# Kernel optimization log

Measured on AMD Instinct MI355X. Metric: run time of the kernel, lower is better.

The kernel has to match this reference:

```python
import jax, jax.numpy as jnp
import numpy as np

B, C, H, W, HEADS = 16, 256, 64, 64, 4
BN_EPS = 1e-5


def setup_inputs() -> dict:
    key = jax.random.key(0)
    ks = jax.random.split(key, 6)
    sc = lambda k, shape, s: (jax.random.normal(k, shape, jnp.float32) * s)
    return {
        "x": sc(ks[0], (B, C, H, W), 1.0),
        "qkv_w": sc(ks[1], (C, C), C ** -0.5),
        "temp": jnp.ones((HEADS, 1), jnp.float32),
        "proj_w": sc(ks[2], (C, C), C ** -0.5),
        "proj_b": jnp.zeros((C,), jnp.float32),
        "conv1_w": sc(ks[3], (2 * C, C), C ** -0.5),
        "bn1_g": jnp.ones((2 * C,), jnp.float32),
        "bn1_b": jnp.zeros((2 * C,), jnp.float32),
        "bn1_m": jnp.zeros((2 * C,), jnp.float32),
        "bn1_v": jnp.ones((2 * C,), jnp.float32),
        "conv2_w": sc(ks[4], (C, 2 * C), (2 * C) ** -0.5),
        "bn2_g": jnp.ones((C,), jnp.float32),
        "bn2_b": jnp.zeros((C,), jnp.float32),
        "bn2_m": jnp.zeros((C,), jnp.float32),
        "bn2_v": jnp.ones((C,), jnp.float32),
    }


def _attention_tssa(x3, qkv_w, temp, proj_w, proj_b):
    # x3: [b, n, c]
    b, n, c = x3.shape
    d = c // HEADS
    w = (x3 @ qkv_w.T).reshape(b, n, HEADS, d).transpose(0, 2, 1, 3)  # b h n d
    # F.normalize over token dim (dim=-2), eps=1e-12
    nrm = jnp.sqrt(jnp.sum(w * w, axis=2, keepdims=True))
    w_normed = w / jnp.maximum(nrm, 1e-12)
    # logits [b, h, n]; temp is (h, 1) -> broadcast per head
    s = jnp.sum(w_normed * w_normed, axis=-1) * temp[:, 0][None, :, None]
    Pi = jax.nn.softmax(s, axis=1)  # softmax over HEAD dim (torch Softmax(dim=1))
    Pi_n = Pi / (jnp.sum(Pi, axis=-1, keepdims=True) + 1e-8)
    dots = jnp.einsum('bhn,bhnd->bhd', Pi_n, w * w)  # [b, h, d]
    attn = 1.0 / (1.0 + dots)
    out = -(w * Pi[..., None]) * attn[:, :, None, :]  # b h n d
    out = out.transpose(0, 2, 1, 3).reshape(b, n, c)
    return out @ proj_w.T + proj_b


def _bn(y, g, b_, m, v):
    scale = (g / jnp.sqrt(v + BN_EPS))[None, :, None, None]
    return (y - m[None, :, None, None]) * scale + b_[None, :, None, None]


def reference(x, qkv_w, temp, proj_w, proj_b, conv1_w, bn1_g, bn1_b, bn1_m, bn1_v,
              conv2_w, bn2_g, bn2_b, bn2_m, bn2_v):
    b, c, h, w_ = x.shape
    x3 = x.reshape(b, c, h * w_).transpose(0, 2, 1)  # b n c
    a = _attention_tssa(x3, qkv_w, temp, proj_w, proj_b)  # b n c
    x = x + a.transpose(0, 2, 1).reshape(b, c, h, w_)
    # FFN: 1x1 conv -> BN -> SiLU -> 1x1 conv -> BN (no act), residual
    y = jnp.einsum('bchw,oc->bohw', x, conv1_w)
    y = _bn(y, bn1_g, bn1_b, bn1_m, bn1_v)
    y = y * jax.nn.sigmoid(y)  # SiLU
    z = jnp.einsum('bchw,oc->bohw', y, conv2_w)
    z = _bn(z, bn2_g, bn2_b, bn2_m, bn2_v)
    return x + z
```

## Files before the change

### kernel.cpp

```cpp
#include <hip/hip_runtime.h>
#include <hip/hip_bf16.h>
#include <stdint.h>

typedef unsigned short u16;
using bf16x8 = __attribute__((ext_vector_type(8))) short;
using f32x4  = __attribute__((ext_vector_type(4))) float;

#define DEVI static __device__ __forceinline__
#define AS1 __attribute__((address_space(1)))
#define AS3 __attribute__((address_space(3)))

constexpr int CB = 16;
constexpr int CC = 256;
constexpr int CN = 4096;
constexpr int CH = 4;

DEVI u16 f2b(float f){
  union { float f; uint32_t u; } v; v.f = f;
  return (u16)((v.u + 0x7FFFu + ((v.u >> 16) & 1u)) >> 16);
}
DEVI float b2f(u16 u){
  union { uint32_t u; float f; } v; v.u = ((uint32_t)u) << 16; return v.f;
}

__global__ __launch_bounds__(256) void k_prep_w(const float* __restrict__ qkv, const float* __restrict__ pj,
    const float* __restrict__ c1, const float* __restrict__ c2,
    u16* __restrict__ qkvb, u16* __restrict__ pjb, u16* __restrict__ c1b, u16* __restrict__ c2b){
  int id = blockIdx.x * 256 + threadIdx.x;
  if (id < 65536) qkvb[id] = f2b(qkv[id]);
  else if (id < 131072) pjb[id - 65536] = f2b(pj[id - 65536]);
  else if (id < 262144) c1b[id - 131072] = f2b(c1[id - 131072]);
  else c2b[id - 262144] = f2b(c2[id - 262144]);
}

__global__ __launch_bounds__(256) void k_prep_bn(const float* __restrict__ g1,const float* __restrict__ b1,
    const float* __restrict__ m1,const float* __restrict__ v1,
    const float* __restrict__ g2,const float* __restrict__ b2,
    const float* __restrict__ m2,const float* __restrict__ v2,
    float* __restrict__ s1,float* __restrict__ o1,float* __restrict__ s2,float* __restrict__ o2){
  int id = blockIdx.x*256 + threadIdx.x;
  if (id < 512){ float s = g1[id] * rsqrtf(v1[id] + 1e-5f); s1[id] = s; o1[id] = b1[id] - m1[id]*s; }
  else if (id < 768){ int c = id - 512; float s = g2[c] * rsqrtf(v2[c] + 1e-5f); s2[c] = s; o2[c] = b2[c] - m2[c]*s; }
}

__global__ __launch_bounds__(256) void k_tr(const float* __restrict__ x, u16* __restrict__ xb){
  __shared__ float t[32][33];
  int b = blockIdx.x, c0 = blockIdx.y*32, n0 = blockIdx.z*32;
  int tr = threadIdx.x >> 5, tc = threadIdx.x & 31;
  const float* xp = x + ((size_t)b*CC + c0)*CN + n0;
  #pragma unroll
  for (int p=0;p<4;p++) t[tr + p*8][tc] = xp[(size_t)(tr + p*8)*CN + tc];
  __syncthreads();
  u16* op = xb + ((size_t)b*CN + n0)*CC + c0;
  #pragma unroll
  for (int p=0;p<4;p++) op[(size_t)(tr + p*8)*CC + tc] = f2b(t[tc][tr + p*8]);
}

template<int M_, int K_, int EPI>
__global__ __launch_bounds__(256) void k_gemm(
    const u16* __restrict__ Aw, const u16* __restrict__ Act,
    float* of, u16* __restrict__ ob,
    const float* __restrict__ e0, const float* __restrict__ e1,
    const u16* __restrict__ eb)
{
  __shared__ __align__(16) u16 As[2][128*64];
  __shared__ __align__(16) u16 Bs[2][128*64];
  const int t = threadIdx.x;
  const int lane = t & 63, wave = t >> 6;
  const int wr = wave >> 1, wc = wave & 1;
  const int lg = lane >> 4, lr = lane & 15;
  const int gx = gridDim.x, gy = gridDim.y;
  const int nwg = gx * gy * gridDim.z;
  const int id0 = blockIdx.x + gx*(blockIdx.y + gy*blockIdx.z);
  const int id  = (id0 & 7)*(nwg >> 3) + (id0 >> 3);
  const int bx = id % gx; const int rem = id / gx;
  const int by = rem % gy; const int bz = rem / gy;
  const int n0 = bx * 128, m0 = by * 128, b = bz;
  const u16* Ag = Aw + (size_t)m0 * K_;
  const u16* Bg = Act + ((size_t)b * CN + n0) * K_;
  f32x4 acc[4][4] = {};
  constexpr int NT = K_/64;
  int goff[4], ldst[4];
  #pragma unroll
  for (int i=0;i<4;i++){
    int off = (i*256 + t) * 8;
    int m = off >> 6, gq = (off >> 3) & 7;
    int kk = (gq ^ (m & 7)) * 8;
    goff[i] = m*K_ + kk;
    ldst[i] = (i*256 + wave*64)*8;
  }
  auto stage = [&](int p, int kt){
    #pragma unroll
    for (int i=0;i<4;i++){
      __builtin_amdgcn_global_load_lds((AS1 void*)(Ag + goff[i] + kt*64),
                                       (AS3 void*)(&As[p][ldst[i]]), 16, 0, 0);
      __builtin_amdgcn_global_load_lds((AS1 void*)(Bg + goff[i] + kt*64),
                                       (AS3 void*)(&Bs[p][ldst[i]]), 16, 0, 0);
    }
  };
  stage(0, 0);
  stage(1, 1);
  for (int kt = 0; kt < NT; ++kt){
    const int cur = kt & 1;
    if (kt + 1 < NT) { asm volatile("s_waitcnt vmcnt(8)" ::: "memory"); }
    else             { asm volatile("s_waitcnt vmcnt(0)" ::: "memory"); }
    __builtin_amdgcn_s_barrier();
    __builtin_amdgcn_sched_barrier(0);
    bf16x8 af[2][4], bfv[2][4];
    #pragma unroll
    for (int s=0;s<2;s++){
      #pragma unroll
      for (int mi=0;mi<4;mi++){
        int r = wr*64 + mi*16 + lr;
        af[s][mi] = *(const bf16x8*)(&As[cur][r*64 + (((s*4+lg) ^ (r & 7)) * 8)]);
        int r2 = wc*64 + mi*16 + lr;
        bfv[s][mi] = *(const bf16x8*)(&Bs[cur][r2*64 + (((s*4+lg) ^ (r2 & 7)) * 8)]);
      }
    }
    asm volatile("s_waitcnt lgkmcnt(0)" ::: "memory");
    __builtin_amdgcn_sched_barrier(0);
    __builtin_amdgcn_s_barrier();
    if (kt + 2 < NT) stage(cur, kt + 2);
    __builtin_amdgcn_s_setprio(1);
    #pragma unroll
    for (int s=0;s<2;s++)
      #pragma unroll
      for (int mi=0;mi<4;mi++)
        #pragma unroll
        for (int ni=0;ni<4;ni++)
          acc[mi][ni] = __builtin_amdgcn_mfma_f32_16x16x32_bf16(af[s][mi], bfv[s][ni], acc[mi][ni], 0, 0, 0);
    __builtin_amdgcn_s_setprio(0);
  }
  #pragma unroll
  for (int mi=0;mi<4;mi++){
    const int mb = m0 + wr*64 + mi*16 + lg*4;
    float sq[4] = {0.f,0.f,0.f,0.f};
    #pragma unroll
    for (int ni=0;ni<4;ni++){
      const int n = n0 + wc*64 + ni*16 + lr;
      f32x4 v = acc[mi][ni];
      if constexpr (EPI == 0){
        ushort4 u;
        #pragma unroll
        for (int j=0;j<4;j++){ ((u16*)&u)[j] = f2b(v[j]); sq[j] += v[j]*v[j]; }
        *(ushort4*)(ob + ((size_t)b*CN + n)*M_ + mb) = u;
      } else if constexpr (EPI == 1){
        ushort4 u;
        #pragma unroll
        for (int j=0;j<4;j++){
          size_t ix = ((size_t)b*CC + mb + j)*CN + n;
          ((u16*)&u)[j] = f2b(v[j] + e0[mb + j] + e1[ix]);
        }
        *(ushort4*)(ob + ((size_t)b*CN + n)*M_ + mb) = u;
      } else if constexpr (EPI == 2){
        ushort4 u;
        #pragma unroll
        for (int j=0;j<4;j++){
          float r = v[j]*e0[mb+j] + e1[mb+j];
          r = r / (1.f + __expf(-r));
          ((u16*)&u)[j] = f2b(r);
        }
        *(ushort4*)(ob + ((size_t)b*CN + n)*M_ + mb) = u;
      } else {
        ushort4 xw = *(const ushort4*)(eb + ((size_t)b*CN + n)*M_ + mb);
        #pragma unroll
        for (int j=0;j<4;j++){
          size_t ix = ((size_t)b*CC + mb + j)*CN + n;
          of[ix] = v[j]*e0[mb+j] + e1[mb+j] + b2f(((const u16*)&xw)[j]);
        }
      }
    }
    if constexpr (EPI == 0){
      #pragma unroll
      for (int off=1; off<16; off<<=1)
        #pragma unroll
        for (int j=0;j<4;j++) sq[j] += __shfl_xor(sq[j], off);
      if (lr == 0){
        #pragma unroll
        for (int j=0;j<4;j++) atomicAdd(&of[b*CC + mb + j], sq[j]);
      }
    }
  }
}

__global__ __launch_bounds__(256) void k_stats(const u16* __restrict__ W, const float* __restrict__ nrm2,
    const float* __restrict__ temp, float* __restrict__ Pi, float* __restrict__ sumPi,
    float* __restrict__ dotsU){
  __shared__ float red[4][256];
  const int b = blockIdx.x, n0 = blockIdx.y * 64;
  const int t = threadIdx.x, lane = t & 63, wave = t >> 6;
  const int grp = lane >> 4, gl = lane & 15;
  const float th = temp[grp];
  const float4 nr = *(const float4*)(nrm2 + b*CC + 4*lane);
  const float i0 = 1.f/fmaxf(nr.x,1e-24f), i1 = 1.f/fmaxf(nr.y,1e-24f);
  const float i2 = 1.f/fmaxf(nr.z,1e-24f), i3 = 1.f/fmaxf(nr.w,1e-24f);
  float accp = 0.f, d0=0.f, d1=0.f, d2=0.f, d3=0.f;
  for (int i=0;i<16;i++){
    int n = n0 + wave*16 + i;
    ushort4 wu = *(const ushort4*)(W + ((size_t)b*CN + n)*CC + 4*lane);
    float w0=b2f(wu.x), w1=b2f(wu.y), w2=b2f(wu.z), w3=b2f(wu.w);
    float q0=w0*w0, q1=w1*w1, q2=w2*w2, q3=w3*w3;
    float s = q0*i0 + q1*i1 + q2*i2 + q3*i3;
    #pragma unroll
    for (int off=1; off<16; off<<=1) s += __shfl_xor(s, off);
    s *= th;
    float sA=__shfl(s,0), sB=__shfl(s,16), sC=__shfl(s,32), sD=__shfl(s,48);
    float mx = fmaxf(fmaxf(sA,sB), fmaxf(sC,sD));
    float eA=__expf(sA-mx), eB=__expf(sB-mx), eC=__expf(sC-mx), eD=__expf(sD-mx);
    float den = eA+eB+eC+eD;
    float pih = ((grp==0)?eA:(grp==1)?eB:(grp==2)?eC:eD)/den;
    if (gl == 0){ Pi[((size_t)b*CH + grp)*CN + n] = pih; accp += pih; }
    d0 += pih*q0; d1 += pih*q1; d2 += pih*q2; d3 += pih*q3;
  }
  if (gl == 0) atomicAdd(&sumPi[b*CH + grp], accp);
  red[wave][4*lane+0]=d0; red[wave][4*lane+1]=d1; red[wave][4*lane+2]=d2; red[wave][4*lane+3]=d3;
  __syncthreads();
  float sm = red[0][t]+red[1][t]+red[2][t]+red[3][t];
  atomicAdd(&dotsU[b*CC + t], sm);
}

__global__ __launch_bounds__(256) void k_outc(const u16* __restrict__ W, const float* __restrict__ Pi,
    const float* __restrict__ dotsU, const float* __restrict__ sumPi, u16* __restrict__ oc){
  size_t id = (size_t)blockIdx.x * 256 + threadIdx.x;
  int c = ((int)(id & 63)) * 4;
  int n = (int)((id >> 6) & (CN - 1));
  int b = (int)(id >> 18);
  int h = c >> 6;
  ushort4 wu = *(const ushort4*)(W + ((size_t)b*CN + n)*CC + c);
  float pi = Pi[((size_t)b*CH + h)*CN + n];
  float sp = sumPi[b*CH + h] + 1e-8f;
  float4 du = *(const float4*)(dotsU + b*CC + c);
  float a0 = sp/(sp + du.x), a1 = sp/(sp + du.y), a2 = sp/(sp + du.z), a3 = sp/(sp + du.w);
  ushort4 u;
  u.x = f2b(-b2f(wu.x) * pi * a0);
  u.y = f2b(-b2f(wu.y) * pi * a1);
  u.z = f2b(-b2f(wu.z) * pi * a2);
  u.w = f2b(-b2f(wu.w) * pi * a3);
  *(ushort4*)(oc + ((size_t)b*CN + n)*CC + c) = u;
}

extern "C" void kernel_launch(void* const* d_in, const int* in_sizes, int n_in,
                              void* d_out, int out_size, void* d_ws, size_t ws_size,
                              hipStream_t stream) {
  (void)in_sizes; (void)n_in; (void)out_size; (void)ws_size;
  const float* x     = (const float*)d_in[0];
  const float* qkvw  = (const float*)d_in[1];
  const float* temp  = (const float*)d_in[2];
  const float* projw = (const float*)d_in[3];
  const float* projb = (const float*)d_in[4];
  const float* c1w   = (const float*)d_in[5];
  const float* g1=(const float*)d_in[6], *b1=(const float*)d_in[7], *m1=(const float*)d_in[8], *v1=(const float*)d_in[9];
  const float* c2w   = (const float*)d_in[10];
  const float* g2=(const float*)d_in[11], *b2=(const float*)d_in[12], *m2=(const float*)d_in[13], *v2=(const float*)d_in[14];
  float* out = (float*)d_out;
  char* ws = (char*)d_ws;

  constexpr size_t MB = 1024*1024;
  u16* xb  = (u16*)(ws);
  u16* oc  = xb;
  u16* yb  = (u16*)(ws);
  u16* xrb = (u16*)(ws + 64*MB);
  u16* Wb  = (u16*)(ws + 96*MB);
  char* wts = ws + 128*MB;
  u16* qkvb = (u16*)wts;
  u16* pjb  = qkvb + 65536;
  u16* c1b  = pjb + 65536;
  u16* c2b  = c1b + 131072;
  float* s1 = (float*)(wts + 786432);
  float* o1 = s1 + 512;
  float* s2 = o1 + 512;
  float* o2 = s2 + 256;
  float* Pi = (float*)(wts + 786432 + 8192);
  float* nrm2  = Pi + (size_t)CB*CH*CN;
  float* sumPi = nrm2 + CB*CC;
  float* dotsU = sumPi + CB*CH;

  hipMemsetAsync(nrm2, 0, (size_t)(CB*CC + CB*CH + CB*CC)*4, stream);
  k_prep_w<<<1536, 256, 0, stream>>>(qkvw, projw, c1w, c2w, qkvb, pjb, c1b, c2b);
  k_prep_bn<<<3, 256, 0, stream>>>(g1,b1,m1,v1,g2,b2,m2,v2,s1,o1,s2,o2);
  k_tr<<<dim3(CB, CC/32, CN/32), 256, 0, stream>>>(x, xb);
  k_gemm<256,256,0><<<dim3(CN/128, 2, CB), 256, 0, stream>>>(qkvb, xb, nrm2, Wb, nullptr, nullptr, nullptr);
  k_stats<<<dim3(CB, CN/64), 256, 0, stream>>>(Wb, nrm2, temp, Pi, sumPi, dotsU);
  k_outc<<<(CB*CN*CC/4)/256, 256, 0, stream>>>(Wb, Pi, dotsU, sumPi, oc);
  k_gemm<256,256,1><<<dim3(CN/128, 2, CB), 256, 0, stream>>>(pjb, oc, nullptr, xrb, projb, x, nullptr);
  k_gemm<512,256,2><<<dim3(CN/128, 4, CB), 256, 0, stream>>>(c1b, xrb, nullptr, yb, s1, o1, nullptr);
  k_gemm<256,512,3><<<dim3(CN/128, 2, CB), 256, 0, stream>>>(c2b, yb, out, nullptr, s2, o2, xrb);
}
```

Before: 216.3 us.

## Stage GEMM epilogue through LDS for coalesced stores; read bf16 residual

For the non-final GEMM epilogues, results are converted to bf16, written into per-wave LDS tiles, then read back and written out as 16-byte nontemporal coalesced stores. This replaces the scattered 8-byte global stores. The projection GEMM now takes its residual from the token-major bf16 copy of x instead of strided fp32 reads of x. To keep that copy intact, the attention output buffer gets its own workspace region. The trade-offs are slightly lower residual precision and extra LDS traffic in the epilogue.

```diff
diff --git a/kernel.cpp b/kernel.cpp
--- a/kernel.cpp
+++ b/kernel.cpp
@@ -5,6 +5,7 @@
 typedef unsigned short u16;
 using bf16x8 = __attribute__((ext_vector_type(8))) short;
 using f32x4  = __attribute__((ext_vector_type(4))) float;
+using u32x4  = __attribute__((ext_vector_type(4))) unsigned int;
 
 #define DEVI static __device__ __forceinline__
 #define AS1 __attribute__((address_space(1)))
@@ -63,8 +64,9 @@
     const float* __restrict__ e0, const float* __restrict__ e1,
     const u16* __restrict__ eb)
 {
-  __shared__ __align__(16) u16 As[2][128*64];
-  __shared__ __align__(16) u16 Bs[2][128*64];
+  __shared__ __align__(16) u16 smem[32768];
+  u16* As = smem;
+  u16* Bs = smem + 16384;
   const int t = threadIdx.x;
   const int lane = t & 63, wave = t >> 6;
   const int wr = wave >> 1, wc = wave & 1;
@@ -93,9 +95,9 @@
     #pragma unroll
     for (int i=0;i<4;i++){
       __builtin_amdgcn_global_load_lds((AS1 void*)(Ag + goff[i] + kt*64),
-                                       (AS3 void*)(&As[p][ldst[i]]), 16, 0, 0);
+                                       (AS3 void*)(As + p*8192 + ldst[i]), 16, 0, 0);
       __builtin_amdgcn_global_load_lds((AS1 void*)(Bg + goff[i] + kt*64),
-                                       (AS3 void*)(&Bs[p][ldst[i]]), 16, 0, 0);
+                                       (AS3 void*)(Bs + p*8192 + ldst[i]), 16, 0, 0);
     }
   };
   stage(0, 0);
@@ -112,9 +114,9 @@
       #pragma unroll
       for (int mi=0;mi<4;mi++){
         int r = wr*64 + mi*16 + lr;
-        af[s][mi] = *(const bf16x8*)(&As[cur][r*64 + (((s*4+lg) ^ (r & 7)) * 8)]);
+        af[s][mi] = *(const bf16x8*)(As + cur*8192 + r*64 + (((s*4+lg) ^ (r & 7)) * 8));
         int r2 = wc*64 + mi*16 + lr;
-        bfv[s][mi] = *(const bf16x8*)(&Bs[cur][r2*64 + (((s*4+lg) ^ (r2 & 7)) * 8)]);
+        bfv[s][mi] = *(const bf16x8*)(Bs + cur*8192 + r2*64 + (((s*4+lg) ^ (r2 & 7)) * 8));
       }
     }
     asm volatile("s_waitcnt lgkmcnt(0)" ::: "memory");
@@ -131,37 +133,14 @@
           acc[mi][ni] = __builtin_amdgcn_mfma_f32_16x16x32_bf16(af[s][mi], bfv[s][ni], acc[mi][ni], 0, 0, 0);
     __builtin_amdgcn_s_setprio(0);
   }
-  #pragma unroll
-  for (int mi=0;mi<4;mi++){
-    const int mb = m0 + wr*64 + mi*16 + lg*4;
-    float sq[4] = {0.f,0.f,0.f,0.f};
-    #pragma unroll
-    for (int ni=0;ni<4;ni++){
-      const int n = n0 + wc*64 + ni*16 + lr;
-      f32x4 v = acc[mi][ni];
-      if constexpr (EPI == 0){
-        ushort4 u;
-        #pragma unroll
-        for (int j=0;j<4;j++){ ((u16*)&u)[j] = f2b(v[j]); sq[j] += v[j]*v[j]; }
-        *(ushort4*)(ob + ((size_t)b*CN + n)*M_ + mb) = u;
-      } else if constexpr (EPI == 1){
-        ushort4 u;
-        #pragma unroll
-        for (int j=0;j<4;j++){
-          size_t ix = ((size_t)b*CC + mb + j)*CN + n;
-          ((u16*)&u)[j] = f2b(v[j] + e0[mb + j] + e1[ix]);
-        }
-        *(ushort4*)(ob + ((size_t)b*CN + n)*M_ + mb) = u;
-      } else if constexpr (EPI == 2){
-        ushort4 u;
-        #pragma unroll
-        for (int j=0;j<4;j++){
-          float r = v[j]*e0[mb+j] + e1[mb+j];
-          r = r / (1.f + __expf(-r));
-          ((u16*)&u)[j] = f2b(r);
-        }
-        *(ushort4*)(ob + ((size_t)b*CN + n)*M_ + mb) = u;
-      } else {
+  if constexpr (EPI == 3){
+    #pragma unroll
+    for (int mi=0;mi<4;mi++){
+      const int mb = m0 + wr*64 + mi*16 + lg*4;
+      #pragma unroll
+      for (int ni=0;ni<4;ni++){
+        const int n = n0 + wc*64 + ni*16 + lr;
+        f32x4 v = acc[mi][ni];
         ushort4 xw = *(const ushort4*)(eb + ((size_t)b*CN + n)*M_ + mb);
         #pragma unroll
         for (int j=0;j<4;j++){
@@ -170,15 +149,56 @@
         }
       }
     }
-    if constexpr (EPI == 0){
+  } else {
+    u16* eps = smem + wave * 4608;
+    #pragma unroll
+    for (int mi=0;mi<4;mi++){
+      const int mb = m0 + wr*64 + mi*16 + lg*4;
+      float sq[4] = {0.f,0.f,0.f,0.f};
       #pragma unroll
-      for (int off=1; off<16; off<<=1)
+      for (int ni=0;ni<4;ni++){
+        const int n = n0 + wc*64 + ni*16 + lr;
+        f32x4 v = acc[mi][ni];
+        ushort4 u;
+        if constexpr (EPI == 0){
+          #pragma unroll
+          for (int j=0;j<4;j++){ ((u16*)&u)[j] = f2b(v[j]); sq[j] += v[j]*v[j]; }
+        } else if constexpr (EPI == 1){
+          ushort4 xw = *(const ushort4*)(eb + ((size_t)b*CN + n)*M_ + mb);
+          #pragma unroll
+          for (int j=0;j<4;j++)
+            ((u16*)&u)[j] = f2b(v[j] + e0[mb + j] + b2f(((const u16*)&xw)[j]));
+        } else {
+          #pragma unroll
+          for (int j=0;j<4;j++){
+            float r = v[j]*e0[mb+j] + e1[mb+j];
+            r = r / (1.f + __expf(-r));
+            ((u16*)&u)[j] = f2b(r);
+          }
+        }
+        *(ushort4*)(eps + (ni*16+lr)*72 + mi*16 + lg*4) = u;
+      }
+      if constexpr (EPI == 0){
         #pragma unroll
-        for (int j=0;j<4;j++) sq[j] += __shfl_xor(sq[j], off);
-      if (lr == 0){
-        #pragma unroll
-        for (int j=0;j<4;j++) atomicAdd(&of[b*CC + mb + j], sq[j]);
+        for (int off=1; off<16; off<<=1)
+          #pragma unroll
+          for (int j=0;j<4;j++) sq[j] += __shfl_xor(sq[j], off);
+        if (lr == 0){
+          #pragma unroll
+          for (int j=0;j<4;j++) atomicAdd(&of[b*CC + mb + j], sq[j]);
+        }
       }
+    }
+    asm volatile("s_waitcnt lgkmcnt(0)" ::: "memory");
+    __builtin_amdgcn_sched_barrier(0);
+    const int mc = lane & 7;
+    #pragma unroll
+    for (int rd=0; rd<8; rd++){
+      const int n_rel = rd*8 + (lane >> 3);
+      u32x4 val = *(const u32x4*)(eps + n_rel*72 + mc*8);
+      const int n = n0 + wc*64 + n_rel;
+      __builtin_nontemporal_store(val,
+          (u32x4*)(ob + ((size_t)b*CN + n)*M_ + m0 + wr*64 + mc*8));
     }
   }
 }
@@ -257,7 +277,7 @@
 
   constexpr size_t MB = 1024*1024;
   u16* xb  = (u16*)(ws);
-  u16* oc  = xb;
+  u16* oc  = (u16*)(ws + 32*MB);
   u16* yb  = (u16*)(ws);
   u16* xrb = (u16*)(ws + 64*MB);
   u16* Wb  = (u16*)(ws + 96*MB);
@@ -282,7 +302,7 @@
   k_gemm<256,256,0><<<dim3(CN/128, 2, CB), 256, 0, stream>>>(qkvb, xb, nrm2, Wb, nullptr, nullptr, nullptr);
   k_stats<<<dim3(CB, CN/64), 256, 0, stream>>>(Wb, nrm2, temp, Pi, sumPi, dotsU);
   k_outc<<<(CB*CN*CC/4)/256, 256, 0, stream>>>(Wb, Pi, dotsU, sumPi, oc);
-  k_gemm<256,256,1><<<dim3(CN/128, 2, CB), 256, 0, stream>>>(pjb, oc, nullptr, xrb, projb, x, nullptr);
+  k_gemm<256,256,1><<<dim3(CN/128, 2, CB), 256, 0, stream>>>(pjb, oc, nullptr, xrb, projb, nullptr, xb);
   k_gemm<512,256,2><<<dim3(CN/128, 4, CB), 256, 0, stream>>>(c1b, xrb, nullptr, yb, s1, o1, nullptr);
   k_gemm<256,512,3><<<dim3(CN/128, 2, CB), 256, 0, stream>>>(c2b, yb, out, nullptr, s2, o2, xrb);
 }
```

New measurement: 226.2 us. 4.6% more time.

## Halve GEMM K-tile to 32 for lower LDS, read residual from bf16 transposed copy

Applied to the files above, without the earlier changes.

Reduces the GEMM K tile from 64 to 32 with a 4-way XOR swizzle. This halves LDS use per block (32KB instead of 64KB), which may allow more resident workgroups, at the cost of twice as many barrier/wait iterations. The projection GEMM epilogue now reads the residual from the bf16 token-major copy of x instead of strided fp32 x. To make that possible, the attention output buffer is moved to a separate workspace region so xb is not overwritten. Using the bf16 residual trades some precision for coalesced, half-width reads.

```diff
diff --git a/kernel.cpp b/kernel.cpp
--- a/kernel.cpp
+++ b/kernel.cpp
@@ -63,8 +63,9 @@
     const float* __restrict__ e0, const float* __restrict__ e1,
     const u16* __restrict__ eb)
 {
-  __shared__ __align__(16) u16 As[2][128*64];
-  __shared__ __align__(16) u16 Bs[2][128*64];
+  __shared__ __align__(16) u16 smem[16384];
+  u16* As = smem;
+  u16* Bs = smem + 8192;
   const int t = threadIdx.x;
   const int lane = t & 63, wave = t >> 6;
   const int wr = wave >> 1, wc = wave & 1;
@@ -79,43 +80,39 @@
   const u16* Ag = Aw + (size_t)m0 * K_;
   const u16* Bg = Act + ((size_t)b * CN + n0) * K_;
   f32x4 acc[4][4] = {};
-  constexpr int NT = K_/64;
-  int goff[4], ldst[4];
-  #pragma unroll
-  for (int i=0;i<4;i++){
+  constexpr int NT = K_/32;
+  int goff[2], ldst[2];
+  #pragma unroll
+  for (int i=0;i<2;i++){
     int off = (i*256 + t) * 8;
-    int m = off >> 6, gq = (off >> 3) & 7;
-    int kk = (gq ^ (m & 7)) * 8;
-    goff[i] = m*K_ + kk;
-    ldst[i] = (i*256 + wave*64)*8;
+    int row = off >> 5, kq = (off >> 3) & 3;
+    goff[i] = row*K_ + (kq ^ (row & 3)) * 8;
+    ldst[i] = off;
   }
   auto stage = [&](int p, int kt){
     #pragma unroll
-    for (int i=0;i<4;i++){
-      __builtin_amdgcn_global_load_lds((AS1 void*)(Ag + goff[i] + kt*64),
-                                       (AS3 void*)(&As[p][ldst[i]]), 16, 0, 0);
-      __builtin_amdgcn_global_load_lds((AS1 void*)(Bg + goff[i] + kt*64),
-                                       (AS3 void*)(&Bs[p][ldst[i]]), 16, 0, 0);
+    for (int i=0;i<2;i++){
+      __builtin_amdgcn_global_load_lds((AS1 void*)(Ag + goff[i] + kt*32),
+                                       (AS3 void*)(As + p*4096 + ldst[i]), 16, 0, 0);
+      __builtin_amdgcn_global_load_lds((AS1 void*)(Bg + goff[i] + kt*32),
+                                       (AS3 void*)(Bs + p*4096 + ldst[i]), 16, 0, 0);
     }
   };
   stage(0, 0);
   stage(1, 1);
   for (int kt = 0; kt < NT; ++kt){
     const int cur = kt & 1;
-    if (kt + 1 < NT) { asm volatile("s_waitcnt vmcnt(8)" ::: "memory"); }
+    if (kt + 1 < NT) { asm volatile("s_waitcnt vmcnt(4)" ::: "memory"); }
     else             { asm volatile("s_waitcnt vmcnt(0)" ::: "memory"); }
     __builtin_amdgcn_s_barrier();
     __builtin_amdgcn_sched_barrier(0);
-    bf16x8 af[2][4], bfv[2][4];
-    #pragma unroll
-    for (int s=0;s<2;s++){
-      #pragma unroll
-      for (int mi=0;mi<4;mi++){
-        int r = wr*64 + mi*16 + lr;
-        af[s][mi] = *(const bf16x8*)(&As[cur][r*64 + (((s*4+lg) ^ (r & 7)) * 8)]);
-        int r2 = wc*64 + mi*16 + lr;
-        bfv[s][mi] = *(const bf16x8*)(&Bs[cur][r2*64 + (((s*4+lg) ^ (r2 & 7)) * 8)]);
-      }
+    bf16x8 af[4], bfv[4];
+    #pragma unroll
+    for (int mi=0;mi<4;mi++){
+      int r = wr*64 + mi*16 + lr;
+      af[mi] = *(const bf16x8*)(As + cur*4096 + r*32 + ((lg ^ (r & 3)) * 8));
+      int r2 = wc*64 + mi*16 + lr;
+      bfv[mi] = *(const bf16x8*)(Bs + cur*4096 + r2*32 + ((lg ^ (r2 & 3)) * 8));
     }
     asm volatile("s_waitcnt lgkmcnt(0)" ::: "memory");
     __builtin_amdgcn_sched_barrier(0);
@@ -123,12 +120,10 @@
     if (kt + 2 < NT) stage(cur, kt + 2);
     __builtin_amdgcn_s_setprio(1);
     #pragma unroll
-    for (int s=0;s<2;s++)
+    for (int mi=0;mi<4;mi++)
       #pragma unroll
-      for (int mi=0;mi<4;mi++)
-        #pragma unroll
-        for (int ni=0;ni<4;ni++)
-          acc[mi][ni] = __builtin_amdgcn_mfma_f32_16x16x32_bf16(af[s][mi], bfv[s][ni], acc[mi][ni], 0, 0, 0);
+      for (int ni=0;ni<4;ni++)
+        acc[mi][ni] = __builtin_amdgcn_mfma_f32_16x16x32_bf16(af[mi], bfv[ni], acc[mi][ni], 0, 0, 0);
     __builtin_amdgcn_s_setprio(0);
   }
   #pragma unroll
@@ -145,12 +140,11 @@
         for (int j=0;j<4;j++){ ((u16*)&u)[j] = f2b(v[j]); sq[j] += v[j]*v[j]; }
         *(ushort4*)(ob + ((size_t)b*CN + n)*M_ + mb) = u;
       } else if constexpr (EPI == 1){
+        ushort4 xw = *(const ushort4*)(eb + ((size_t)b*CN + n)*M_ + mb);
         ushort4 u;
         #pragma unroll
-        for (int j=0;j<4;j++){
-          size_t ix = ((size_t)b*CC + mb + j)*CN + n;
-          ((u16*)&u)[j] = f2b(v[j] + e0[mb + j] + e1[ix]);
-        }
+        for (int j=0;j<4;j++)
+          ((u16*)&u)[j] = f2b(v[j] + e0[mb + j] + b2f(((const u16*)&xw)[j]));
         *(ushort4*)(ob + ((size_t)b*CN + n)*M_ + mb) = u;
       } else if constexpr (EPI == 2){
         ushort4 u;
@@ -257,7 +251,7 @@
 
   constexpr size_t MB = 1024*1024;
   u16* xb  = (u16*)(ws);
-  u16* oc  = xb;
+  u16* oc  = (u16*)(ws + 32*MB);
   u16* yb  = (u16*)(ws);
   u16* xrb = (u16*)(ws + 64*MB);
   u16* Wb  = (u16*)(ws + 96*MB);
@@ -282,7 +276,7 @@
   k_gemm<256,256,0><<<dim3(CN/128, 2, CB), 256, 0, stream>>>(qkvb, xb, nrm2, Wb, nullptr, nullptr, nullptr);
   k_stats<<<dim3(CB, CN/64), 256, 0, stream>>>(Wb, nrm2, temp, Pi, sumPi, dotsU);
   k_outc<<<(CB*CN*CC/4)/256, 256, 0, stream>>>(Wb, Pi, dotsU, sumPi, oc);
-  k_gemm<256,256,1><<<dim3(CN/128, 2, CB), 256, 0, stream>>>(pjb, oc, nullptr, xrb, projb, x, nullptr);
+  k_gemm<256,256,1><<<dim3(CN/128, 2, CB), 256, 0, stream>>>(pjb, oc, nullptr, xrb, projb, nullptr, xb);
   k_gemm<512,256,2><<<dim3(CN/128, 4, CB), 256, 0, stream>>>(c1b, xrb, nullptr, yb, s1, o1, nullptr);
   k_gemm<256,512,3><<<dim3(CN/128, 2, CB), 256, 0, stream>>>(c2b, yb, out, nullptr, s2, o2, xrb);
 }
```

Result: slower. 242.7 us (+12.2%).

## Fuse FFN conv1+BN+SiLU+conv2 into one kernel keeping hidden tile in LDS

Applied to the files above, without the earlier changes.

Adds a k_ffn kernel that, for each 128-token tile, computes the 512-channel hidden activation with BN and SiLU, stores it swizzled in LDS, and then runs the second 1x1 conv plus BN and residual from LDS. This removes the global round trip of the hidden tensor and one kernel launch. The projection epilogue now adds the residual from the bf16 transposed x instead of strided fp32 x, so the residual carries bf16 rounding. The fused kernel uses about 160KB of LDS, so each CU runs one workgroup and occupancy is lower, and the first GEMM's A tiles are restreamed per token tile.

```diff
diff --git a/kernel.cpp b/kernel.cpp
--- a/kernel.cpp
+++ b/kernel.cpp
@@ -60,8 +60,7 @@
 __global__ __launch_bounds__(256) void k_gemm(
     const u16* __restrict__ Aw, const u16* __restrict__ Act,
     float* of, u16* __restrict__ ob,
-    const float* __restrict__ e0, const float* __restrict__ e1,
-    const u16* __restrict__ eb)
+    const float* __restrict__ e0, const u16* __restrict__ eb)
 {
   __shared__ __align__(16) u16 As[2][128*64];
   __shared__ __align__(16) u16 Bs[2][128*64];
@@ -144,40 +143,179 @@
         #pragma unroll
         for (int j=0;j<4;j++){ ((u16*)&u)[j] = f2b(v[j]); sq[j] += v[j]*v[j]; }
         *(ushort4*)(ob + ((size_t)b*CN + n)*M_ + mb) = u;
-      } else if constexpr (EPI == 1){
-        ushort4 u;
-        #pragma unroll
-        for (int j=0;j<4;j++){
-          size_t ix = ((size_t)b*CC + mb + j)*CN + n;
-          ((u16*)&u)[j] = f2b(v[j] + e0[mb + j] + e1[ix]);
-        }
-        *(ushort4*)(ob + ((size_t)b*CN + n)*M_ + mb) = u;
-      } else if constexpr (EPI == 2){
-        ushort4 u;
-        #pragma unroll
-        for (int j=0;j<4;j++){
-          float r = v[j]*e0[mb+j] + e1[mb+j];
-          r = r / (1.f + __expf(-r));
-          ((u16*)&u)[j] = f2b(r);
-        }
-        *(ushort4*)(ob + ((size_t)b*CN + n)*M_ + mb) = u;
       } else {
         ushort4 xw = *(const ushort4*)(eb + ((size_t)b*CN + n)*M_ + mb);
-        #pragma unroll
-        for (int j=0;j<4;j++){
-          size_t ix = ((size_t)b*CC + mb + j)*CN + n;
-          of[ix] = v[j]*e0[mb+j] + e1[mb+j] + b2f(((const u16*)&xw)[j]);
+        ushort4 u;
+        #pragma unroll
+        for (int j=0;j<4;j++)
+          ((u16*)&u)[j] = f2b(v[j] + e0[mb + j] + b2f(((const u16*)&xw)[j]));
+        *(ushort4*)(ob + ((size_t)b*CN + n)*M_ + mb) = u;
+      }
+    }
+    if constexpr (EPI == 0){
+      #pragma unroll
+      for (int off=1; off<16; off<<=1)
+        #pragma unroll
+        for (int j=0;j<4;j++) sq[j] += __shfl_xor(sq[j], off);
+      if (lr == 0){
+        #pragma unroll
+        for (int j=0;j<4;j++) atomicAdd(&of[b*CC + mb + j], sq[j]);
+      }
+    }
+  }
+}
+
+__global__ __launch_bounds__(256, 1) void k_ffn(
+    const u16* __restrict__ Xr, const u16* __restrict__ W1, const u16* __restrict__ W2,
+    const float* __restrict__ s1, const float* __restrict__ o1,
+    const float* __restrict__ s2, const float* __restrict__ o2,
+    float* __restrict__ out)
+{
+  __shared__ __align__(16) u16 smem[81920];
+  u16* As = smem;
+  u16* Bs = smem + 8192;
+  u16* Y  = smem + 16384;
+  const int t = threadIdx.x, lane = t & 63, wave = t >> 6;
+  const int wr = wave >> 1, wc = wave & 1, lg = lane >> 4, lr = lane & 15;
+  const int nb = gridDim.x * gridDim.y;
+  const int id0 = blockIdx.x + gridDim.x * blockIdx.y;
+  const int id  = (id0 & 7)*(nb >> 3) + (id0 >> 3);
+  const int n0 = (id % gridDim.x) * 128, b = id / gridDim.x;
+  const u16* Bg = Xr + ((size_t)b*CN + n0)*CC;
+  int srow[2], skq[2], ldst[2];
+  #pragma unroll
+  for (int i=0;i<2;i++){
+    int off = (i*256 + t) * 8;
+    srow[i] = off >> 5; skq[i] = (off >> 3) & 3; ldst[i] = off;
+  }
+  auto stA1 = [&](int p, int f){
+    int mp = f >> 3, kt = f & 7;
+    #pragma unroll
+    for (int i=0;i<2;i++)
+      __builtin_amdgcn_global_load_lds(
+        (AS1 void*)(W1 + (size_t)(mp*128 + srow[i])*256 + kt*32 + ((skq[i] ^ (srow[i]&3))*8)),
+        (AS3 void*)(As + p*4096 + ldst[i]), 16, 0, 0);
+  };
+  auto stB1 = [&](int p, int f){
+    int kt = f & 7;
+    #pragma unroll
+    for (int i=0;i<2;i++)
+      __builtin_amdgcn_global_load_lds(
+        (AS1 void*)(Bg + (size_t)srow[i]*256 + kt*32 + ((skq[i] ^ (srow[i]&3))*8)),
+        (AS3 void*)(Bs + p*4096 + ldst[i]), 16, 0, 0);
+  };
+  auto stA2 = [&](int p, int f){
+    int mp2 = f >> 4, kt2 = f & 15;
+    #pragma unroll
+    for (int i=0;i<2;i++)
+      __builtin_amdgcn_global_load_lds(
+        (AS1 void*)(W2 + (size_t)(mp2*128 + srow[i])*512 + kt2*32 + ((skq[i] ^ (srow[i]&3))*8)),
+        (AS3 void*)(As + p*4096 + ldst[i]), 16, 0, 0);
+  };
+  f32x4 acc[4][4] = {};
+  stA1(0,0); stB1(0,0); stA1(1,1); stB1(1,1);
+  for (int f = 0; f < 32; ++f){
+    const int cur = f & 1;
+    if (f + 1 < 32) { asm volatile("s_waitcnt vmcnt(4)" ::: "memory"); }
+    else            { asm volatile("s_waitcnt vmcnt(0)" ::: "memory"); }
+    __builtin_amdgcn_s_barrier();
+    __builtin_amdgcn_sched_barrier(0);
+    bf16x8 af[4], bv[4];
+    #pragma unroll
+    for (int mi=0;mi<4;mi++){
+      int r = wr*64 + mi*16 + lr;
+      af[mi] = *(const bf16x8*)(As + cur*4096 + r*32 + ((lg ^ (r & 3)) * 8));
+      int r2 = wc*64 + mi*16 + lr;
+      bv[mi] = *(const bf16x8*)(Bs + cur*4096 + r2*32 + ((lg ^ (r2 & 3)) * 8));
+    }
+    asm volatile("s_waitcnt lgkmcnt(0)" ::: "memory");
+    __builtin_amdgcn_sched_barrier(0);
+    __builtin_amdgcn_s_barrier();
+    if (f + 2 < 32){ stA1(cur, f+2); stB1(cur, f+2); }
+    __builtin_amdgcn_s_setprio(1);
+    #pragma unroll
+    for (int mi=0;mi<4;mi++)
+      #pragma unroll
+      for (int ni=0;ni<4;ni++)
+        acc[mi][ni] = __builtin_amdgcn_mfma_f32_16x16x32_bf16(af[mi], bv[ni], acc[mi][ni], 0, 0, 0);
+    __builtin_amdgcn_s_setprio(0);
+    if ((f & 7) == 7){
+      const int mp = f >> 3;
+      #pragma unroll
+      for (int mi=0;mi<4;mi++){
+        const int m_rel = wr*64 + mi*16 + lg*4;
+        const int mg = mp*128 + m_rel;
+        #pragma unroll
+        for (int ni=0;ni<4;ni++){
+          const int n_rel = wc*64 + ni*16 + lr;
+          ushort4 u;
+          #pragma unroll
+          for (int j=0;j<4;j++){
+            float r = acc[mi][ni][j]*s1[mg+j] + o1[mg+j];
+            r = r / (1.f + __expf(-r));
+            ((u16*)&u)[j] = f2b(r);
+          }
+          const int qm = mg >> 3;
+          *(ushort4*)(Y + n_rel*512 + ((qm ^ (n_rel & 7))*8) + (mg & 7)) = u;
+          acc[mi][ni] = (f32x4){0.f,0.f,0.f,0.f};
         }
       }
     }
-    if constexpr (EPI == 0){
-      #pragma unroll
-      for (int off=1; off<16; off<<=1)
-        #pragma unroll
-        for (int j=0;j<4;j++) sq[j] += __shfl_xor(sq[j], off);
-      if (lr == 0){
-        #pragma unroll
-        for (int j=0;j<4;j++) atomicAdd(&of[b*CC + mb + j], sq[j]);
+  }
+  asm volatile("s_waitcnt lgkmcnt(0)" ::: "memory");
+  __builtin_amdgcn_sched_barrier(0);
+  __builtin_amdgcn_s_barrier();
+  f32x4 a2[2][4][4] = {};
+  stA2(0,0); stA2(1,1);
+  for (int f = 0; f < 32; ++f){
+    const int cur = f & 1;
+    if (f + 1 < 32) { asm volatile("s_waitcnt vmcnt(2)" ::: "memory"); }
+    else            { asm volatile("s_waitcnt vmcnt(0)" ::: "memory"); }
+    __builtin_amdgcn_s_barrier();
+    __builtin_amdgcn_sched_barrier(0);
+    bf16x8 af[4], bv[4];
+    const int kt2 = f & 15;
+    #pragma unroll
+    for (int mi=0;mi<4;mi++){
+      int r = wr*64 + mi*16 + lr;
+      af[mi] = *(const bf16x8*)(As + cur*4096 + r*32 + ((lg ^ (r & 3)) * 8));
+      int n_rel = wc*64 + mi*16 + lr;
+      int qm = kt2*4 + lg;
+      bv[mi] = *(const bf16x8*)(Y + n_rel*512 + ((qm ^ (n_rel & 7))*8));
+    }
+    asm volatile("s_waitcnt lgkmcnt(0)" ::: "memory");
+    __builtin_amdgcn_sched_barrier(0);
+    __builtin_amdgcn_s_barrier();
+    if (f + 2 < 32) stA2(cur, f+2);
+    __builtin_amdgcn_s_setprio(1);
+    if (f < 16){
+      #pragma unroll
+      for (int mi=0;mi<4;mi++)
+        #pragma unroll
+        for (int ni=0;ni<4;ni++)
+          a2[0][mi][ni] = __builtin_amdgcn_mfma_f32_16x16x32_bf16(af[mi], bv[ni], a2[0][mi][ni], 0, 0, 0);
+    } else {
+      #pragma unroll
+      for (int mi=0;mi<4;mi++)
+        #pragma unroll
+        for (int ni=0;ni<4;ni++)
+          a2[1][mi][ni] = __builtin_amdgcn_mfma_f32_16x16x32_bf16(af[mi], bv[ni], a2[1][mi][ni], 0, 0, 0);
+    }
+    __builtin_amdgcn_s_setprio(0);
+  }
+  #pragma unroll
+  for (int p2=0;p2<2;p2++){
+    #pragma unroll
+    for (int mi=0;mi<4;mi++){
+      const int c = p2*128 + wr*64 + mi*16 + lg*4;
+      #pragma unroll
+      for (int ni=0;ni<4;ni++){
+        const int n = n0 + wc*64 + ni*16 + lr;
+        ushort4 xw = *(const ushort4*)(Xr + ((size_t)b*CN + n)*CC + c);
+        #pragma unroll
+        for (int j=0;j<4;j++)
+          out[((size_t)b*CC + c + j)*CN + n] =
+            a2[p2][mi][ni][j]*s2[c+j] + o2[c+j] + b2f(((const u16*)&xw)[j]);
       }
     }
   }
@@ -257,8 +395,7 @@
 
   constexpr size_t MB = 1024*1024;
   u16* xb  = (u16*)(ws);
-  u16* oc  = xb;
-  u16* yb  = (u16*)(ws);
+  u16* oc  = (u16*)(ws + 32*MB);
   u16* xrb = (u16*)(ws + 64*MB);
   u16* Wb  = (u16*)(ws + 96*MB);
   char* wts = ws + 128*MB;
@@ -279,10 +416,9 @@
   k_prep_w<<<1536, 256, 0, stream>>>(qkvw, projw, c1w, c2w, qkvb, pjb, c1b, c2b);
   k_prep_bn<<<3, 256, 0, stream>>>(g1,b1,m1,v1,g2,b2,m2,v2,s1,o1,s2,o2);
   k_tr<<<dim3(CB, CC/32, CN/32), 256, 0, stream>>>(x, xb);
-  k_gemm<256,256,0><<<dim3(CN/128, 2, CB), 256, 0, stream>>>(qkvb, xb, nrm2, Wb, nullptr, nullptr, nullptr);
+  k_gemm<256,256,0><<<dim3(CN/128, 2, CB), 256, 0, stream>>>(qkvb, xb, nrm2, Wb, nullptr, nullptr);
   k_stats<<<dim3(CB, CN/64), 256, 0, stream>>>(Wb, nrm2, temp, Pi, sumPi, dotsU);
   k_outc<<<(CB*CN*CC/4)/256, 256, 0, stream>>>(Wb, Pi, dotsU, sumPi, oc);
-  k_gemm<256,256,1><<<dim3(CN/128, 2, CB), 256, 0, stream>>>(pjb, oc, nullptr, xrb, projb, x, nullptr);
-  k_gemm<512,256,2><<<dim3(CN/128, 4, CB), 256, 0, stream>>>(c1b, xrb, nullptr, yb, s1, o1, nullptr);
-  k_gemm<256,512,3><<<dim3(CN/128, 2, CB), 256, 0, stream>>>(c2b, yb, out, nullptr, s2, o2, xrb);
-}
+  k_gemm<256,256,1><<<dim3(CN/128, 2, CB), 256, 0, stream>>>(pjb, oc, nullptr, xrb, projb, xb);
+  k_ffn<<<dim3(CN/128, CB), 256, 0, stream>>>(xrb, c1b, c2b, s1, o1, s2, o2, out);
+}
```

Result: slower. 262.3 us (+21.3%).
